# Kernel tuning notes

Hardware: AMD Instinct MI355X
Metric: run time of the kernel (lower is better)

The kernel has to match this reference:

```python
import jax, jax.numpy as jnp
import numpy as np

RAD = 4   # corr lookup radius
NH, NP = 8, 4  # deform attn heads / points (single level)


def conv2d(x, w, b, pad):
    y = jax.lax.conv_general_dilated(x, w, (1, 1), [(pad, pad), (pad, pad)],
                                     dimension_numbers=('NCHW', 'OIHW', 'NCHW'))
    return y + b[None, :, None, None]


def bilinear_gather(imgf, H, W, px, py):
    # imgf: [N, C, H*W]; px, py: [N, P] pixel coords; zero padding (grid_sample 'zeros')
    x0 = jnp.floor(px); y0 = jnp.floor(py)
    wx = px - x0; wy = py - y0
    def tap(xi, yi, wt):
        valid = (xi >= 0) & (xi <= W - 1) & (yi >= 0) & (yi <= H - 1)
        idx = (jnp.clip(yi, 0, H - 1) * W + jnp.clip(xi, 0, W - 1)).astype(jnp.int32)
        v = jnp.take_along_axis(imgf, idx[:, None, :], axis=2)
        return v * (wt * valid)[:, None, :]
    return (tap(x0, y0, (1 - wx) * (1 - wy)) + tap(x0 + 1, y0, wx * (1 - wy))
            + tap(x0, y0 + 1, (1 - wx) * wy) + tap(x0 + 1, y0 + 1, wx * wy))


def sine_pos_embed(B, H, W, npf, temperature=10000.0):
    # PositionEmbeddingSine with normalize=True
    scale = 2.0 * np.pi; eps = 1e-6
    y = jnp.broadcast_to(jnp.arange(1, H + 1, dtype=jnp.float32)[:, None], (H, W))
    x = jnp.broadcast_to(jnp.arange(1, W + 1, dtype=jnp.float32)[None, :], (H, W))
    y = (y - 0.5) / (H + eps) * scale
    x = (x - 0.5) / (W + eps) * scale
    dim_t = temperature ** (2.0 * (jnp.arange(npf) // 2).astype(jnp.float32) / npf)
    px = x[..., None] / dim_t
    py = y[..., None] / dim_t
    px = jnp.stack([jnp.sin(px[..., 0::2]), jnp.cos(px[..., 1::2])], -1).reshape(H, W, npf)
    py = jnp.stack([jnp.sin(py[..., 0::2]), jnp.cos(py[..., 1::2])], -1).reshape(H, W, npf)
    pos = jnp.concatenate([py, px], -1)
    return jnp.broadcast_to(pos[None], (B, H, W, 2 * npf)).reshape(B, H * W, 2 * npf)


def layer_norm(x, g, b):
    m = x.mean(-1, keepdims=True)
    v = ((x - m) ** 2).mean(-1, keepdims=True)
    return (x - m) / jnp.sqrt(v + 1e-5) * g + b


def _forward(fmap1, fmap2, flow, wc1, bc1, wc2, bc2, wf1, bf1, wf2, bf2, wcf, bcf,
             wfh1, bfh1, wfh2, bfh2, w_off, b_off, w_aw, b_aw, w_val, b_val,
             w_out, b_out, ln1_g, ln1_b, w_ff1, b_ff1, w_ff2, b_ff2, ln2_g, ln2_b):
    B, C, H, W = fmap1.shape
    HW = H * W
    dh = C // NH
    relu = jax.nn.relu
    # ---- CorrBlock.corr: all-pairs correlation volume ----
    corr = jnp.einsum('bcq,bck->bqk', fmap1.reshape(B, C, HW), fmap2.reshape(B, C, HW))
    corr = corr / jnp.sqrt(jnp.asarray(C, jnp.float32))
    corrf = corr.reshape(B * HW, 1, HW)  # [B*HW, 1, H2*W2]
    # ---- correlation lookup at coords = base grid + flow (bilinear, align_corners=True) ----
    gy, gx = jnp.meshgrid(jnp.arange(H, dtype=jnp.float32),
                          jnp.arange(W, dtype=jnp.float32), indexing='ij')
    cx = (gx[None] + flow[:, 0]).reshape(B * HW)
    cy = (gy[None] + flow[:, 1]).reshape(B * HW)
    d = jnp.linspace(-RAD, RAD, 2 * RAD + 1)
    oy, ox = jnp.meshgrid(d, d, indexing='ij')  # RAFT quirk: delta[...,0]=dy, delta[...,1]=dx
    px = cx[:, None] + oy.reshape(-1)[None, :]
    py = cy[:, None] + ox.reshape(-1)[None, :]
    corr_feat = bilinear_gather(corrf, H, W, px, py).reshape(B, H, W, (2 * RAD + 1) ** 2)
    corr_feat = corr_feat.transpose(0, 3, 1, 2)  # [B, 81, H, W]
    # ---- BasicMotionEncoder + FlowHead (BasicUpdateBlock.forward path) ----
    cor = relu(conv2d(corr_feat, wc1, bc1, 0))
    cor = relu(conv2d(cor, wc2, bc2, 1))
    flo = relu(conv2d(flow, wf1, bf1, 3))
    flo = relu(conv2d(flo, wf2, bf2, 1))
    mf = relu(conv2d(jnp.concatenate([cor, flo], 1), wcf, bcf, 1))
    mf = jnp.concatenate([mf, flow], 1)  # [B,128,H,W]
    delta_flow = conv2d(relu(conv2d(mf, wfh1, bfh1, 1)), wfh2, bfh2, 1)  # [B,2,H,W]
    # ---- single-level MSDeformAttn encoder layer over fmap1 tokens ----
    src = fmap1.reshape(B, C, HW).transpose(0, 2, 1)  # [B, Lq, C]
    pos = sine_pos_embed(B, H, W, C // 2)
    q = src + pos
    off = (q @ w_off.T + b_off).reshape(B, HW, NH, 1, NP, 2)
    aw = jax.nn.softmax((q @ w_aw.T + b_aw).reshape(B, HW, NH, NP), axis=-1)
    val = (src @ w_val.T + b_val).reshape(B, HW, NH, dh)
    ref = jnp.stack([(gx.reshape(-1) + 0.5) / W, (gy.reshape(-1) + 0.5) / H], -1)  # [HW,2]
    loc = (ref[None, :, None, None, None, :] + off / jnp.asarray([W, H], jnp.float32))[:, :, :, 0]
    # normalized loc -> pixel coords with align_corners=False convention
    px2 = (loc[..., 0] * W - 0.5).transpose(0, 2, 1, 3).reshape(B * NH, HW * NP)
    py2 = (loc[..., 1] * H - 0.5).transpose(0, 2, 1, 3).reshape(B * NH, HW * NP)
    vflat = val.transpose(0, 2, 3, 1).reshape(B * NH, dh, HW)
    samp = bilinear_gather(vflat, H, W, px2, py2).reshape(B, NH, dh, HW, NP)
    attn = (samp * aw.transpose(0, 2, 1, 3)[:, :, None]).sum(-1)  # [B,NH,dh,HW]
    attn = attn.transpose(0, 3, 1, 2).reshape(B, HW, C) @ w_out.T + b_out
    src = layer_norm(src + attn, ln1_g, ln1_b)
    ff = jax.nn.relu(src @ w_ff1.T + b_ff1) @ w_ff2.T + b_ff2
    src = layer_norm(src + ff, ln2_g, ln2_b)
    return src, delta_flow


def setup_inputs():
    key = jax.random.key(0)
    ks = jax.random.split(key, 20)
    B, C, H, W = 4, 256, 48, 48
    def w(i, shape, s=0.02):
        return jax.random.normal(ks[i], shape, jnp.float32) * s
    return {
        'fmap1': jax.random.normal(ks[0], (B, C, H, W), jnp.float32),
        'fmap2': jax.random.normal(ks[1], (B, C, H, W), jnp.float32),
        'flow': jax.random.normal(ks[2], (B, 2, H, W), jnp.float32),
        'wc1': w(3, (256, 81, 1, 1)), 'bc1': jnp.zeros((256,)),
        'wc2': w(4, (192, 256, 3, 3)), 'bc2': jnp.zeros((192,)),
        'wf1': w(5, (128, 2, 7, 7)), 'bf1': jnp.zeros((128,)),
        'wf2': w(6, (64, 128, 3, 3)), 'bf2': jnp.zeros((64,)),
        'wcf': w(7, (126, 256, 3, 3)), 'bcf': jnp.zeros((126,)),
        'wfh1': w(8, (256, 128, 3, 3)), 'bfh1': jnp.zeros((256,)),
        'wfh2': w(9, (2, 256, 3, 3)), 'bfh2': jnp.zeros((2,)),
        'w_off': w(10, (64, 256)), 'b_off': jnp.zeros((64,)),
        'w_aw': w(11, (32, 256)), 'b_aw': jnp.zeros((32,)),
        'w_val': w(12, (256, 256)), 'b_val': jnp.zeros((256,)),
        'w_out': w(13, (256, 256)), 'b_out': jnp.zeros((256,)),
        'ln1_g': jnp.ones((256,)), 'ln1_b': jnp.zeros((256,)),
        'w_ff1': w(14, (1024, 256)), 'b_ff1': jnp.zeros((1024,)),
        'w_ff2': w(15, (256, 1024)), 'b_ff2': jnp.zeros((256,)),
        'ln2_g': jnp.ones((256,)), 'ln2_b': jnp.zeros((256,)),
    }


def reference(fmap1, fmap2, flow, wc1, bc1, wc2, bc2, wf1, bf1, wf2, bf2, wcf, bcf,
              wfh1, bfh1, wfh2, bfh2, w_off, b_off, w_aw, b_aw, w_val, b_val,
              w_out, b_out, ln1_g, ln1_b, w_ff1, b_ff1, w_ff2, b_ff2, ln2_g, ln2_b):
    return _forward(fmap1, fmap2, flow, wc1, bc1, wc2, bc2, wf1, bf1, wf2, bf2, wcf, bcf,
                    wfh1, bfh1, wfh2, bfh2, w_off, b_off, w_aw, b_aw, w_val, b_val,
                    w_out, b_out, ln1_g, ln1_b, w_ff1, b_ff1, w_ff2, b_ff2, ln2_g, ln2_b)
```

## Files before the change

### kernel.cpp

```cpp
#include <hip/hip_runtime.h>
#include <hip/hip_bf16.h>
#include <math.h>

#define HH 48
#define WW 48
#define HW 2304
#define BB 4
#define CC 256

typedef __hip_bfloat16 bf16;
typedef __attribute__((ext_vector_type(8))) short s8v;
typedef __attribute__((ext_vector_type(4))) float f4v;

__device__ inline float bf2f(short u) {
  unsigned v = ((unsigned)(unsigned short)u) << 16;
  return __builtin_bit_cast(float, v);
}

__global__ __launch_bounds__(256) void prep_k(const float* __restrict__ fmap1,
                                              const float* __restrict__ fmap2,
                                              float* __restrict__ srcT,
                                              bf16* __restrict__ f1t,
                                              bf16* __restrict__ qb,
                                              bf16* __restrict__ f2t) {
  __shared__ float t[64][65];
  int z = blockIdx.z;
  int p0 = blockIdx.x * 64, c0 = blockIdx.y * 64;
  int b = z & 3;
  const float* src = (z < 4) ? fmap2 : fmap1;
  const float* inb = src + ((size_t)b * CC + c0) * HW + p0;
#pragma unroll
  for (int i = 0; i < 16; ++i) {
    int idx = threadIdx.x + i * 256;
    int c = idx >> 6, p = idx & 63;
    t[c][p] = inb[(size_t)c * HW + p];
  }
  __syncthreads();
  if (z < 4) {
    bf16* ob = f2t + ((size_t)b * HW + p0) * 256 + c0;
#pragma unroll
    for (int i = 0; i < 16; ++i) {
      int idx = threadIdx.x + i * 256;
      int p = idx >> 6, c = idx & 63;
      ob[(size_t)p * 256 + c] = (bf16)t[c][p];
    }
  } else {
    const float TWO_PI = 6.283185307179586f;
#pragma unroll
    for (int i = 0; i < 16; ++i) {
      int idx = threadIdx.x + i * 256;
      int pl = idx >> 6, cl = idx & 63;
      int c = c0 + cl;
      int p = p0 + pl;
      int y = p / WW, x = p % WW;
      float s = t[cl][pl];
      int axis = c >> 7;
      int cc = c & 127;
      int mm = cc >> 1;
      float coord = (axis ? ((float)x + 0.5f) : ((float)y + 0.5f)) * (TWO_PI / (48.f + 1e-6f));
      float tp = exp2f((float)mm * (13.287712379549449f / 64.f));
      float a = coord / tp;
      float pv = (cc & 1) ? cosf(a) : sinf(a);
      size_t o = ((size_t)b * HW + p) * 256 + c;
      srcT[o] = s;
      f1t[o] = (bf16)s;
      qb[o] = (bf16)(s + pv);
    }
  }
}

__global__ __launch_bounds__(256) void fused_corr_k(const bf16* __restrict__ f1t,
                                                    const bf16* __restrict__ f2t,
                                                    const float* __restrict__ flow,
                                                    bf16* __restrict__ cf) {
  __shared__ float Dls[4][112];
  int wave = threadIdx.x >> 6, lane = threadIdx.x & 63;
  int q = blockIdx.x * 4 + wave;
  int b = q / HW, p = q - b * HW;
  int y = p / WW, x = p - y * WW;
  float fx = flow[((size_t)b * 2 + 0) * HW + p];
  float fy = flow[((size_t)b * 2 + 1) * HW + p];
  float sx = (float)x + fx, sy = (float)y + fy;
  float fx0 = floorf(sx), fy0 = floorf(sy);
  int ix0 = (int)fx0, iy0 = (int)fy0;
  float wx = sx - fx0, wy = sy - fy0;
  int fl = lane & 15, fk8 = lane >> 4;
  s8v bfrag[8];
  const bf16* f1q = f1t + (size_t)q * 256;
#pragma unroll
  for (int ks = 0; ks < 8; ++ks) bfrag[ks] = *(const s8v*)(f1q + ks * 32 + fk8 * 8);
  const bf16* rowp[7];
#pragma unroll
  for (int g = 0; g < 7; ++g) {
    int w = g * 16 + fl;
    int jy = w / 10, jx = w - jy * 10;
    int ky = iy0 - 4 + jy, kx = ix0 - 4 + jx;
    bool valid = (w < 100) && ((unsigned)kx < (unsigned)WW) && ((unsigned)ky < (unsigned)HH);
    rowp[g] = valid ? (f2t + ((size_t)b * HW + ky * WW + kx) * 256) : nullptr;
  }
  f4v acc[7] = {};
#pragma unroll
  for (int g = 0; g < 7; ++g) {
#pragma unroll
    for (int ks = 0; ks < 8; ++ks) {
      s8v a = {0, 0, 0, 0, 0, 0, 0, 0};
      if (rowp[g]) a = *(const s8v*)(rowp[g] + ks * 32 + fk8 * 8);
      acc[g] = __builtin_amdgcn_mfma_f32_16x16x32_bf16(a, bfrag[ks], acc[g], 0, 0, 0);
    }
  }
  if (fl == 0) {
#pragma unroll
    for (int g = 0; g < 7; ++g)
#pragma unroll
      for (int r = 0; r < 4; ++r)
        Dls[wave][g * 16 + fk8 * 4 + r] = acc[g][r] * 0.0625f;
  }
  __syncthreads();
  float w00 = (1.f - wx) * (1.f - wy), w10 = wx * (1.f - wy);
  float w01 = (1.f - wx) * wy, w11 = wx * wy;
  const float* D = Dls[wave];
  bf16* cfr = cf + (size_t)q * 96;
  for (int t = lane; t < 96; t += 64) {
    float v = 0.f;
    if (t < 81) {
      int jx = t / 9, jy = t - jx * 9;
      v = w00 * D[jy * 10 + jx] + w10 * D[jy * 10 + jx + 1] +
          w01 * D[(jy + 1) * 10 + jx] + w11 * D[(jy + 1) * 10 + jx + 1];
    }
    cfr[t] = (bf16)v;
  }
}

struct WtSegs {
  const float* src[12];
  unsigned dstOff[12];
  int Cout[12], Cin[12], KP[12], KS2[12];
  unsigned cum[13];
};

__global__ __launch_bounds__(256) void wt_all_k(WtSegs s, bf16* __restrict__ base) {
  unsigned idx = blockIdx.x * 256 + threadIdx.x;
  if (idx >= s.cum[12]) return;
  int seg = 0;
#pragma unroll
  for (int i = 1; i < 12; ++i)
    if (idx >= s.cum[i]) seg = i;
  unsigned r = idx - s.cum[seg];
  int KP = s.KP[seg], Cout = s.Cout[seg], Cin = s.Cin[seg], KS2 = s.KS2[seg];
  int c = r % KP;
  int o = (r / KP) % Cout;
  int t = r / (KP * Cout);
  float v;
  if (KS2 == 0) {
    int cc = c >> 6, tt = c & 63;
    v = (tt < 49) ? s.src[seg][((size_t)o * 2 + cc) * 49 + tt] : 0.f;
  } else {
    v = (c < Cin) ? s.src[seg][((size_t)o * Cin + c) * KS2 + t] : 0.f;
  }
  base[s.dstOff[seg] + r] = (bf16)v;
}

__global__ __launch_bounds__(256) void im2col7_k(const float* __restrict__ flow,
                                                 bf16* __restrict__ col7) {
  int g = blockIdx.x * 256 + threadIdx.x;
  int kp = g & 127;
  int n = g >> 7;
  int b = n / HW;
  int p = n % HW;
  int y = p / WW, x = p % WW;
  int cc = kp >> 6, tt = kp & 63;
  float v = 0.f;
  if (tt < 49) {
    int ky = tt / 7, kx = tt % 7;
    int yy = y + ky - 3, xx = x + kx - 3;
    if ((unsigned)yy < (unsigned)HH && (unsigned)xx < (unsigned)WW)
      v = flow[((size_t)b * 2 + cc) * HW + yy * WW + xx];
  }
  col7[g] = (bf16)v;
}

struct GSegs {
  const bf16* in[4];
  const bf16* wt[4];
  const float* bias[4];
  const float* bias2[4];
  float* outf[4];
  bf16* outb[4];
  int split[4], O[4], KP[4], taps[4], OStride[4], OOff[4], relu[4], nTn[4];
  int blkStart[4];
  int nseg;
};

__global__ __launch_bounds__(256) void gemm_group_k(GSegs s) {
  int blk = blockIdx.x;
  int seg = 0;
#pragma unroll
  for (int i = 1; i < 4; ++i)
    if (i < s.nseg && blk >= s.blkStart[i]) seg = i;
  int rel = blk - s.blkStart[seg];
  int nTn = s.nTn[seg];
  int bm = rel / nTn, bn = rel % nTn;
  int m0 = bm * 128, n0 = bn * 64;
  int KP = s.KP[seg], O = s.O[seg], taps = s.taps[seg];
  const bf16* in = s.in[seg];
  const bf16* wt = s.wt[seg];

  __shared__ short As[2][128][64];
  __shared__ short Bs[2][64][64];
  int tid = threadIdx.x;
  int arl = tid >> 1, asl = (tid & 1) * 4;
  int brl = tid >> 2, bsl = (tid & 3) * 2;
  int wave = tid >> 6, lane = tid & 63;
  int wm = (wave >> 1) * 64, wn = (wave & 1) * 32;
  int fl = lane & 15, fk8 = lane >> 4;
  f4v acc[4][2] = {};
  int m = m0 + arl;
  int b = m / HW;
  int p = m - b * HW;
  int y = p / WW, x = p - y * WW;
  int wo = n0 + brl;
  bool wvalid = wo < O;
  int wo_c = wvalid ? wo : 0;

  int nc0 = (KP + 63) >> 6;
  int S = taps * nc0;
  uint4 apre[4], bpre[2];

  auto load_stage = [&](int st) {
    int t = st / nc0;
    int c0 = (st - t * nc0) * 64;
    int yy = y, xx = x;
    bool valid = true;
    if (taps == 9) {
      int ky = t / 3, kx = t - ky * 3;
      yy = y + ky - 1;
      xx = x + kx - 1;
      valid = ((unsigned)yy < (unsigned)HH) & ((unsigned)xx < (unsigned)WW);
    }
    const bf16* arow = in + ((size_t)b * HW + yy * WW + xx) * KP;
    const bf16* wrow = wt + ((size_t)t * O + wo_c) * KP;
#pragma unroll
    for (int q = 0; q < 4; ++q) {
      int col = c0 + (asl + q) * 8;
      uint4 v = {0u, 0u, 0u, 0u};
      if (valid && col < KP) v = *(const uint4*)(arow + col);
      apre[q] = v;
    }
#pragma unroll
    for (int q = 0; q < 2; ++q) {
      int col = c0 + (bsl + q) * 8;
      uint4 v = {0u, 0u, 0u, 0u};
      if (wvalid && col < KP) v = *(const uint4*)(wrow + col);
      bpre[q] = v;
    }
  };

  load_stage(0);
  int cur = 0;
  for (int st = 0; st < S; ++st) {
#pragma unroll
    for (int q = 0; q < 4; ++q) {
      int sr = asl + q;
      *(uint4*)&As[cur][arl][((sr ^ (arl & 7))) * 8] = apre[q];
    }
#pragma unroll
    for (int q = 0; q < 2; ++q) {
      int sr = bsl + q;
      *(uint4*)&Bs[cur][brl][((sr ^ (brl & 7))) * 8] = bpre[q];
    }
    if (st + 1 < S) load_stage(st + 1);
    __syncthreads();
#pragma unroll
    for (int cc = 0; cc < 2; ++cc) {
      s8v af[4], bfr[2];
#pragma unroll
      for (int i = 0; i < 4; ++i) {
        int ar = wm + i * 16 + fl;
        af[i] = *(const s8v*)&As[cur][ar][(((cc * 4 + fk8) ^ (ar & 7))) * 8];
      }
#pragma unroll
      for (int j = 0; j < 2; ++j) {
        int br = wn + j * 16 + fl;
        bfr[j] = *(const s8v*)&Bs[cur][br][(((cc * 4 + fk8) ^ (br & 7))) * 8];
      }
#pragma unroll
      for (int i = 0; i < 4; ++i)
#pragma unroll
        for (int j = 0; j < 2; ++j)
          acc[i][j] = __builtin_amdgcn_mfma_f32_16x16x32_bf16(af[i], bfr[j], acc[i][j], 0, 0, 0);
    }
    cur ^= 1;
  }
  int OStride = s.OStride[seg], OOff = s.OOff[seg], relu = s.relu[seg], split = s.split[seg];
  const float* bias = s.bias[seg];
  const float* bias2 = s.bias2[seg];
  float* outf = s.outf[seg];
  bf16* outb = s.outb[seg];
#pragma unroll
  for (int j = 0; j < 2; ++j) {
    int o = n0 + wn + j * 16 + fl;
    if (o < O) {
      float bsv = (bias2 != nullptr && o >= split) ? bias2[o - split] : bias[o];
#pragma unroll
      for (int i = 0; i < 4; ++i)
#pragma unroll
        for (int r = 0; r < 4; ++r) {
          int mm = m0 + wm + i * 16 + fk8 * 4 + r;
          float v = acc[i][j][r] + bsv;
          if (relu) v = fmaxf(v, 0.f);
          if (outb) outb[(size_t)mm * OStride + OOff + o] = (bf16)v;
          else outf[(size_t)mm * OStride + OOff + o] = v;
        }
    }
  }
}

__global__ __launch_bounds__(256) void convfh2_k(const bf16* __restrict__ fh1,
                                                 const float* __restrict__ w,
                                                 const float* __restrict__ bias,
                                                 float* __restrict__ out) {
  __shared__ float wl[4608];
  int tid = threadIdx.x;
#pragma unroll
  for (int i = tid; i < 4608; i += 256) {
    int o2 = i & 1;
    int t = (i >> 1) % 9;
    int c = i / 18;
    wl[i] = w[((size_t)o2 * 256 + c) * 9 + t];
  }
  __syncthreads();
  int wave = tid >> 6, lane = tid & 63;
  int pix = blockIdx.x * 4 + wave;
  int b = pix / HW;
  int q = pix % HW;
  int y = q / WW, x = q % WW;
  int c0 = lane * 4;
  float a0 = 0.f, a1 = 0.f;
#pragma unroll
  for (int ky = 0; ky < 3; ++ky) {
    int yy = y + ky - 1;
    if ((unsigned)yy >= (unsigned)HH) continue;
#pragma unroll
    for (int kx = 0; kx < 3; ++kx) {
      int xx = x + kx - 1;
      if ((unsigned)xx >= (unsigned)WW) continue;
      int t = ky * 3 + kx;
      const bf16* row = fh1 + ((size_t)b * HW + yy * WW + xx) * 256 + c0;
      ushort4 v = *(const ushort4*)row;
      unsigned short vv[4] = {v.x, v.y, v.z, v.w};
#pragma unroll
      for (int j = 0; j < 4; ++j) {
        float fv = bf2f((short)vv[j]);
        float2 wp = *(const float2*)&wl[((c0 + j) * 9 + t) * 2];
        a0 += fv * wp.x;
        a1 += fv * wp.y;
      }
    }
  }
#pragma unroll
  for (int offl = 32; offl > 0; offl >>= 1) {
    a0 += __shfl_xor(a0, offl);
    a1 += __shfl_xor(a1, offl);
  }
  if (lane == 0) {
    out[(size_t)b * 2 * HW + q] = a0 + bias[0];
    out[((size_t)b * 2 + 1) * HW + q] = a1 + bias[1];
  }
}

__global__ void copy_flow_k(const float* __restrict__ flow, bf16* __restrict__ mf) {
  int g = blockIdx.x * 256 + threadIdx.x;
  int p = g % HW;
  int c = (g / HW) % 2;
  int b = g / (2 * HW);
  mf[((size_t)b * HW + p) * 128 + 126 + c] = (bf16)flow[g];
}

__global__ __launch_bounds__(256) void deform_k(const float* __restrict__ val,
                                                const float* __restrict__ oa,
                                                bf16* __restrict__ attn) {
  int g = blockIdx.x * 256 + threadIdx.x;
  int d = g & 31;
  int nh = g >> 5;
  int h = nh & 7;
  int n = nh >> 3;
  int b = n / HW;
  int p = n % HW;
  int y = p / WW, x = p % WW;
  const float* ap = oa + (size_t)n * 96 + 64 + h * 4;
  float l0 = ap[0], l1 = ap[1], l2 = ap[2], l3 = ap[3];
  float mx = fmaxf(fmaxf(l0, l1), fmaxf(l2, l3));
  float e0 = expf(l0 - mx), e1 = expf(l1 - mx), e2 = expf(l2 - mx), e3 = expf(l3 - mx);
  float inv = 1.f / (e0 + e1 + e2 + e3);
  float wts[4] = {e0 * inv, e1 * inv, e2 * inv, e3 * inv};
  const float* offp = oa + (size_t)n * 96 + h * 8;
  const float* vb = val + (size_t)b * HW * 256 + h * 32 + d;
  float acc = 0.f;
#pragma unroll
  for (int pt = 0; pt < 4; ++pt) {
    float ox = offp[pt * 2 + 0];
    float oy = offp[pt * 2 + 1];
    float w = wts[pt];
    float px = (float)x + ox, py = (float)y + oy;
    float x0f = floorf(px), y0f = floorf(py);
    int x0 = (int)x0f, y0 = (int)y0f;
    float wx = px - x0f, wy = py - y0f;
    float s = 0.f;
    if ((unsigned)x0 < WW && (unsigned)y0 < HH)
      s += vb[(size_t)(y0 * WW + x0) * 256] * (1.f - wx) * (1.f - wy);
    if ((unsigned)(x0 + 1) < WW && (unsigned)y0 < HH)
      s += vb[(size_t)(y0 * WW + x0 + 1) * 256] * wx * (1.f - wy);
    if ((unsigned)x0 < WW && (unsigned)(y0 + 1) < HH)
      s += vb[(size_t)((y0 + 1) * WW + x0) * 256] * (1.f - wx) * wy;
    if ((unsigned)(x0 + 1) < WW && (unsigned)(y0 + 1) < HH)
      s += vb[(size_t)((y0 + 1) * WW + x0 + 1) * 256] * wx * wy;
    acc += w * s;
  }
  attn[(size_t)n * 256 + h * 32 + d] = (bf16)acc;
}

__global__ __launch_bounds__(256) void ln_add_k(const float* __restrict__ A,
                                                const float* __restrict__ Bv,
                                                const float* __restrict__ g,
                                                const float* __restrict__ be,
                                                float* __restrict__ out,
                                                bf16* __restrict__ outb) {
  int n = blockIdx.x;
  int c = threadIdx.x;
  float v = A[(size_t)n * 256 + c] + Bv[(size_t)n * 256 + c];
  float s1 = v, s2 = v * v;
#pragma unroll
  for (int o = 32; o > 0; o >>= 1) {
    s1 += __shfl_down(s1, o);
    s2 += __shfl_down(s2, o);
  }
  __shared__ float r1[4], r2[4], mv[2];
  int wid = c >> 6, lane = c & 63;
  if (lane == 0) {
    r1[wid] = s1;
    r2[wid] = s2;
  }
  __syncthreads();
  if (c == 0) {
    float a = r1[0] + r1[1] + r1[2] + r1[3];
    float q2 = r2[0] + r2[1] + r2[2] + r2[3];
    float mean = a * (1.f / 256.f);
    mv[0] = mean;
    mv[1] = q2 * (1.f / 256.f) - mean * mean;
  }
  __syncthreads();
  float mean = mv[0], var = mv[1];
  float r = (v - mean) * rsqrtf(var + 1e-5f) * g[c] + be[c];
  out[(size_t)n * 256 + c] = r;
  if (outb) outb[(size_t)n * 256 + c] = (bf16)r;
}

extern "C" void kernel_launch(void* const* d_in, const int* in_sizes, int n_in,
                              void* d_out, int out_size, void* d_ws, size_t ws_size,
                              hipStream_t stream) {
  const float* fmap1 = (const float*)d_in[0];
  const float* fmap2 = (const float*)d_in[1];
  const float* flow = (const float*)d_in[2];
  const float* wc1 = (const float*)d_in[3];
  const float* bc1 = (const float*)d_in[4];
  const float* wc2 = (const float*)d_in[5];
  const float* bc2 = (const float*)d_in[6];
  const float* wf1 = (const float*)d_in[7];
  const float* bf1 = (const float*)d_in[8];
  const float* wf2 = (const float*)d_in[9];
  const float* bf2 = (const float*)d_in[10];
  const float* wcf = (const float*)d_in[11];
  const float* bcf = (const float*)d_in[12];
  const float* wfh1 = (const float*)d_in[13];
  const float* bfh1 = (const float*)d_in[14];
  const float* wfh2 = (const float*)d_in[15];
  const float* bfh2 = (const float*)d_in[16];
  const float* w_off = (const float*)d_in[17];
  const float* b_off = (const float*)d_in[18];
  const float* w_aw = (const float*)d_in[19];
  const float* b_aw = (const float*)d_in[20];
  const float* w_val = (const float*)d_in[21];
  const float* b_val = (const float*)d_in[22];
  const float* w_out = (const float*)d_in[23];
  const float* b_out = (const float*)d_in[24];
  const float* ln1_g = (const float*)d_in[25];
  const float* ln1_b = (const float*)d_in[26];
  const float* w_ff1 = (const float*)d_in[27];
  const float* b_ff1 = (const float*)d_in[28];
  const float* w_ff2 = (const float*)d_in[29];
  const float* b_ff2 = (const float*)d_in[30];
  const float* ln2_g = (const float*)d_in[31];
  const float* ln2_b = (const float*)d_in[32];

  float* ws = (float*)d_ws;
  float* out_src = (float*)d_out;
  float* out_df = out_src + (size_t)BB * HW * CC;

  const size_t F_WT = 0;
  const size_t F_F1T = 11700000;
  const size_t F_F2T = 12900000;
  const size_t F_QB = 14100000;
  const size_t F_SRCT = 15300000;
  const size_t F_CF = 17700000;
  const size_t F_COL7 = 18200000;
  const size_t F_COR1 = 18800000;
  const size_t F_FLO1 = 20000000;
  const size_t F_CAT = 20600000;
  const size_t F_MF = 21800000;
  const size_t F_FH1 = 22400000;
  const size_t F_OA = 23600000;
  const size_t F_VAL = 24500000;
  const size_t F_ATTN = 26900000;
  const size_t F_TMP = 28100000;
  const size_t F_SRC1 = 30500000;
  const size_t F_SRC1B = 32900000;
  const size_t F_FF1 = 34100000;
  const size_t F_FF2 = 38900000;

  bf16* wkbase = (bf16*)(ws + F_WT);
  bf16* wk1 = wkbase + 0;
  bf16* wk2 = wkbase + 24576;
  bf16* wkf2 = wkbase + 466944;
  bf16* wkcf = wkbase + 540672;
  bf16* wkfh1 = wkbase + 830976;
  bf16* wl_oa = wkbase + 1125888;
  bf16* wl_val = wkbase + 1150464;
  bf16* wl_out = wkbase + 1216000;
  bf16* wl_ff1 = wkbase + 1281536;
  bf16* wl_ff2 = wkbase + 1543680;
  bf16* wk7 = wkbase + 1805824;
  bf16* f1t = (bf16*)(ws + F_F1T);
  bf16* f2t = (bf16*)(ws + F_F2T);
  bf16* qb = (bf16*)(ws + F_QB);
  bf16* cf = (bf16*)(ws + F_CF);
  bf16* col7 = (bf16*)(ws + F_COL7);
  bf16* cor1 = (bf16*)(ws + F_COR1);
  bf16* flo1 = (bf16*)(ws + F_FLO1);
  bf16* cat = (bf16*)(ws + F_CAT);
  bf16* mf = (bf16*)(ws + F_MF);
  bf16* fh1 = (bf16*)(ws + F_FH1);
  bf16* attnb = (bf16*)(ws + F_ATTN);
  bf16* src1b = (bf16*)(ws + F_SRC1B);
  bf16* ff1b = (bf16*)(ws + F_FF1);

  WtSegs segs;
  const float* srcs[12] = {wc1, wc2, wf2, wcf, wfh1, w_off, w_aw, w_val, w_out, w_ff1, w_ff2, wf1};
  unsigned offs[12] = {0, 24576, 466944, 540672, 830976, 1125888, 1142272, 1150464, 1216000, 1281536, 1543680, 1805824};
  int couts[12] = {256, 192, 64, 126, 256, 64, 32, 256, 256, 1024, 256, 128};
  int cins[12] = {81, 256, 128, 256, 128, 256, 256, 256, 256, 256, 1024, 2};
  int kps[12] = {96, 256, 128, 256, 128, 256, 256, 256, 256, 256, 1024, 128};
  int ks2[12] = {1, 9, 9, 9, 9, 1, 1, 1, 1, 1, 1, 0};
  unsigned cum = 0;
  for (int i = 0; i < 12; ++i) {
    segs.src[i] = srcs[i];
    segs.dstOff[i] = offs[i];
    segs.Cout[i] = couts[i];
    segs.Cin[i] = cins[i];
    segs.KP[i] = kps[i];
    segs.KS2[i] = ks2[i];
    segs.cum[i] = cum;
    cum += (unsigned)((ks2[i] ? ks2[i] : 1) * couts[i] * kps[i]);
  }
  segs.cum[12] = cum;
  wt_all_k<<<dim3((cum + 255) / 256), 256, 0, stream>>>(segs, wkbase);

  prep_k<<<dim3(36, 4, 8), 256, 0, stream>>>(fmap1, fmap2, ws + F_SRCT, f1t, qb, f2t);
  im2col7_k<<<dim3(4608), 256, 0, stream>>>(flow, col7);
  copy_flow_k<<<dim3(72), 256, 0, stream>>>(flow, mf);

  fused_corr_k<<<dim3(2304), 256, 0, stream>>>(f1t, f2t, flow, cf);

  auto setseg = [](GSegs& G, int i, const bf16* in, const bf16* wt, const float* bias,
                   const float* bias2, int split, float* outf, bf16* outb, int O, int KP,
                   int taps, int OStride, int OOff, int relu) {
    G.in[i] = in; G.wt[i] = wt; G.bias[i] = bias; G.bias2[i] = bias2; G.split[i] = split;
    G.outf[i] = outf; G.outb[i] = outb; G.O[i] = O; G.KP[i] = KP; G.taps[i] = taps;
    G.OStride[i] = OStride; G.OOff[i] = OOff; G.relu[i] = relu;
    G.nTn[i] = (O + 63) / 64;
  };
  auto finseg = [](GSegs& G, int n) {
    int cumb = 0;
    for (int i = 0; i < 4; ++i) {
      if (i < n) { G.blkStart[i] = cumb; cumb += G.nTn[i] * 72; }
      else G.blkStart[i] = 0x7fffffff;
    }
    G.nseg = n;
    return cumb;
  };

  GSegs GA;
  setseg(GA, 0, cf, wk1, bc1, nullptr, 1 << 30, nullptr, cor1, 256, 96, 1, 256, 0, 1);
  setseg(GA, 1, col7, wk7, bf1, nullptr, 1 << 30, nullptr, flo1, 128, 128, 1, 128, 0, 1);
  setseg(GA, 2, qb, wl_oa, b_off, b_aw, 64, ws + F_OA, nullptr, 96, 256, 1, 96, 0, 0);
  setseg(GA, 3, f1t, wl_val, b_val, nullptr, 1 << 30, ws + F_VAL, nullptr, 256, 256, 1, 256, 0, 0);
  int nblkA = finseg(GA, 4);
  gemm_group_k<<<dim3(nblkA), 256, 0, stream>>>(GA);

  deform_k<<<dim3(9216), 256, 0, stream>>>(ws + F_VAL, ws + F_OA, attnb);

  GSegs GB;
  setseg(GB, 0, cor1, wk2, bc2, nullptr, 1 << 30, nullptr, cat, 192, 256, 9, 256, 0, 1);
  setseg(GB, 1, flo1, wkf2, bf2, nullptr, 1 << 30, nullptr, cat, 64, 128, 9, 256, 192, 1);
  setseg(GB, 2, attnb, wl_out, b_out, nullptr, 1 << 30, ws + F_TMP, nullptr, 256, 256, 1, 256, 0, 0);
  int nblkB = finseg(GB, 3);
  gemm_group_k<<<dim3(nblkB), 256, 0, stream>>>(GB);

  ln_add_k<<<dim3(9216), 256, 0, stream>>>(ws + F_TMP, ws + F_SRCT, ln1_g, ln1_b, ws + F_SRC1, src1b);

  GSegs GC;
  setseg(GC, 0, cat, wkcf, bcf, nullptr, 1 << 30, nullptr, mf, 126, 256, 9, 128, 0, 1);
  setseg(GC, 1, src1b, wl_ff1, b_ff1, nullptr, 1 << 30, nullptr, ff1b, 1024, 256, 1, 1024, 0, 1);
  int nblkC = finseg(GC, 2);
  gemm_group_k<<<dim3(nblkC), 256, 0, stream>>>(GC);

  GSegs GD;
  setseg(GD, 0, mf, wkfh1, bfh1, nullptr, 1 << 30, nullptr, fh1, 256, 128, 9, 256, 0, 1);
  setseg(GD, 1, ff1b, wl_ff2, b_ff2, nullptr, 1 << 30, ws + F_FF2, nullptr, 256, 1024, 1, 256, 0, 0);
  int nblkD = finseg(GD, 2);
  gemm_group_k<<<dim3(nblkD), 256, 0, stream>>>(GD);

  convfh2_k<<<dim3(2304), 256, 0, stream>>>(fh1, wfh2, bfh2, out_df);
  ln_add_k<<<dim3(9216), 256, 0, stream>>>(ws + F_FF2, ws + F_SRC1, ln2_g, ln2_b, out_src, nullptr);

  (void)in_sizes; (void)n_in; (void)out_size; (void)ws_size;
}
```

Baseline: 277.1 us.

## Fold correlation into grouped GEMM launch and reschedule GEMM segments across stages

Removes the standalone correlation kernel and appends its blocks to the first grouped GEMM launch, so the corr lookup runs concurrently with the flow conv, offset/attention and value projections. The corr1 GEMM moves to the second launch, and the grouped GEMMs are regrouped into five launches following the dependency chain. The corr inner loop is also changed to double-buffer its f2 fragment loads ahead of the MFMAs. The extra launch and the uneven mix of block types within a launch may offset the gain from the overlap.

```diff
diff --git a/kernel.cpp b/kernel.cpp
--- a/kernel.cpp
+++ b/kernel.cpp
@@ -69,68 +69,6 @@
   }
 }
 
-__global__ __launch_bounds__(256) void fused_corr_k(const bf16* __restrict__ f1t,
-                                                    const bf16* __restrict__ f2t,
-                                                    const float* __restrict__ flow,
-                                                    bf16* __restrict__ cf) {
-  __shared__ float Dls[4][112];
-  int wave = threadIdx.x >> 6, lane = threadIdx.x & 63;
-  int q = blockIdx.x * 4 + wave;
-  int b = q / HW, p = q - b * HW;
-  int y = p / WW, x = p - y * WW;
-  float fx = flow[((size_t)b * 2 + 0) * HW + p];
-  float fy = flow[((size_t)b * 2 + 1) * HW + p];
-  float sx = (float)x + fx, sy = (float)y + fy;
-  float fx0 = floorf(sx), fy0 = floorf(sy);
-  int ix0 = (int)fx0, iy0 = (int)fy0;
-  float wx = sx - fx0, wy = sy - fy0;
-  int fl = lane & 15, fk8 = lane >> 4;
-  s8v bfrag[8];
-  const bf16* f1q = f1t + (size_t)q * 256;
-#pragma unroll
-  for (int ks = 0; ks < 8; ++ks) bfrag[ks] = *(const s8v*)(f1q + ks * 32 + fk8 * 8);
-  const bf16* rowp[7];
-#pragma unroll
-  for (int g = 0; g < 7; ++g) {
-    int w = g * 16 + fl;
-    int jy = w / 10, jx = w - jy * 10;
-    int ky = iy0 - 4 + jy, kx = ix0 - 4 + jx;
-    bool valid = (w < 100) && ((unsigned)kx < (unsigned)WW) && ((unsigned)ky < (unsigned)HH);
-    rowp[g] = valid ? (f2t + ((size_t)b * HW + ky * WW + kx) * 256) : nullptr;
-  }
-  f4v acc[7] = {};
-#pragma unroll
-  for (int g = 0; g < 7; ++g) {
-#pragma unroll
-    for (int ks = 0; ks < 8; ++ks) {
-      s8v a = {0, 0, 0, 0, 0, 0, 0, 0};
-      if (rowp[g]) a = *(const s8v*)(rowp[g] + ks * 32 + fk8 * 8);
-      acc[g] = __builtin_amdgcn_mfma_f32_16x16x32_bf16(a, bfrag[ks], acc[g], 0, 0, 0);
-    }
-  }
-  if (fl == 0) {
-#pragma unroll
-    for (int g = 0; g < 7; ++g)
-#pragma unroll
-      for (int r = 0; r < 4; ++r)
-        Dls[wave][g * 16 + fk8 * 4 + r] = acc[g][r] * 0.0625f;
-  }
-  __syncthreads();
-  float w00 = (1.f - wx) * (1.f - wy), w10 = wx * (1.f - wy);
-  float w01 = (1.f - wx) * wy, w11 = wx * wy;
-  const float* D = Dls[wave];
-  bf16* cfr = cf + (size_t)q * 96;
-  for (int t = lane; t < 96; t += 64) {
-    float v = 0.f;
-    if (t < 81) {
-      int jx = t / 9, jy = t - jx * 9;
-      v = w00 * D[jy * 10 + jx] + w10 * D[jy * 10 + jx + 1] +
-          w01 * D[(jy + 1) * 10 + jx] + w11 * D[(jy + 1) * 10 + jx + 1];
-    }
-    cfr[t] = (bf16)v;
-  }
-}
-
 struct WtSegs {
   const float* src[12];
   unsigned dstOff[12];
@@ -191,7 +129,86 @@
   int nseg;
 };
 
-__global__ __launch_bounds__(256) void gemm_group_k(GSegs s) {
+__global__ __launch_bounds__(256) void mega_k(GSegs s, int corrStart,
+                                              const bf16* __restrict__ f1t,
+                                              const bf16* __restrict__ f2t,
+                                              const float* __restrict__ flow,
+                                              bf16* __restrict__ cf) {
+  __shared__ short As[2][128][64];
+  __shared__ short Bs[2][64][64];
+
+  if ((int)blockIdx.x >= corrStart) {
+    int cb = blockIdx.x - corrStart;
+    int wave = threadIdx.x >> 6, lane = threadIdx.x & 63;
+    int q = cb * 4 + wave;
+    int b = q / HW, p = q - b * HW;
+    int y = p / WW, x = p - y * WW;
+    float fx = flow[((size_t)b * 2 + 0) * HW + p];
+    float fy = flow[((size_t)b * 2 + 1) * HW + p];
+    float sx = (float)x + fx, sy = (float)y + fy;
+    float fx0 = floorf(sx), fy0 = floorf(sy);
+    int ix0 = (int)fx0, iy0 = (int)fy0;
+    float wx = sx - fx0, wy = sy - fy0;
+    int fl = lane & 15, fk8 = lane >> 4;
+    s8v bfrag[8];
+    const bf16* f1q = f1t + (size_t)q * 256;
+#pragma unroll
+    for (int ks = 0; ks < 8; ++ks) bfrag[ks] = *(const s8v*)(f1q + ks * 32 + fk8 * 8);
+    const bf16* rowp[7];
+#pragma unroll
+    for (int g = 0; g < 7; ++g) {
+      int w = g * 16 + fl;
+      int jy = w / 10, jx = w - jy * 10;
+      int ky = iy0 - 4 + jy, kx = ix0 - 4 + jx;
+      bool valid = (w < 100) && ((unsigned)kx < (unsigned)WW) && ((unsigned)ky < (unsigned)HH);
+      rowp[g] = valid ? (f2t + ((size_t)b * HW + ky * WW + kx) * 256) : nullptr;
+    }
+    f4v acc[7] = {};
+    s8v af[2][7];
+#pragma unroll
+    for (int g = 0; g < 7; ++g) {
+      s8v a = {0, 0, 0, 0, 0, 0, 0, 0};
+      if (rowp[g]) a = *(const s8v*)(rowp[g] + fk8 * 8);
+      af[0][g] = a;
+    }
+#pragma unroll
+    for (int ks = 0; ks < 8; ++ks) {
+      if (ks < 7) {
+#pragma unroll
+        for (int g = 0; g < 7; ++g) {
+          s8v a = {0, 0, 0, 0, 0, 0, 0, 0};
+          if (rowp[g]) a = *(const s8v*)(rowp[g] + (ks + 1) * 32 + fk8 * 8);
+          af[(ks + 1) & 1][g] = a;
+        }
+      }
+#pragma unroll
+      for (int g = 0; g < 7; ++g)
+        acc[g] = __builtin_amdgcn_mfma_f32_16x16x32_bf16(af[ks & 1][g], bfrag[ks], acc[g], 0, 0, 0);
+    }
+    float* Dls = ((float*)As) + wave * 112;
+    if (fl == 0) {
+#pragma unroll
+      for (int g = 0; g < 7; ++g)
+#pragma unroll
+        for (int r = 0; r < 4; ++r)
+          Dls[g * 16 + fk8 * 4 + r] = acc[g][r] * 0.0625f;
+    }
+    __syncthreads();
+    float w00 = (1.f - wx) * (1.f - wy), w10 = wx * (1.f - wy);
+    float w01 = (1.f - wx) * wy, w11 = wx * wy;
+    bf16* cfr = cf + (size_t)q * 96;
+    for (int t = lane; t < 96; t += 64) {
+      float v = 0.f;
+      if (t < 81) {
+        int jx = t / 9, jy = t - jx * 9;
+        v = w00 * Dls[jy * 10 + jx] + w10 * Dls[jy * 10 + jx + 1] +
+            w01 * Dls[(jy + 1) * 10 + jx] + w11 * Dls[(jy + 1) * 10 + jx + 1];
+      }
+      cfr[t] = (bf16)v;
+    }
+    return;
+  }
+
   int blk = blockIdx.x;
   int seg = 0;
 #pragma unroll
@@ -205,8 +222,6 @@
   const bf16* in = s.in[seg];
   const bf16* wt = s.wt[seg];
 
-  __shared__ short As[2][128][64];
-  __shared__ short Bs[2][64][64];
   int tid = threadIdx.x;
   int arl = tid >> 1, asl = (tid & 1) * 4;
   int brl = tid >> 2, bsl = (tid & 3) * 2;
@@ -272,11 +287,11 @@
     __syncthreads();
 #pragma unroll
     for (int cc = 0; cc < 2; ++cc) {
-      s8v af[4], bfr[2];
+      s8v af2[4], bfr[2];
 #pragma unroll
       for (int i = 0; i < 4; ++i) {
         int ar = wm + i * 16 + fl;
-        af[i] = *(const s8v*)&As[cur][ar][(((cc * 4 + fk8) ^ (ar & 7))) * 8];
+        af2[i] = *(const s8v*)&As[cur][ar][(((cc * 4 + fk8) ^ (ar & 7))) * 8];
       }
 #pragma unroll
       for (int j = 0; j < 2; ++j) {
@@ -287,7 +302,7 @@
       for (int i = 0; i < 4; ++i)
 #pragma unroll
         for (int j = 0; j < 2; ++j)
-          acc[i][j] = __builtin_amdgcn_mfma_f32_16x16x32_bf16(af[i], bfr[j], acc[i][j], 0, 0, 0);
+          acc[i][j] = __builtin_amdgcn_mfma_f32_16x16x32_bf16(af2[i], bfr[j], acc[i][j], 0, 0, 0);
     }
     cur ^= 1;
   }
@@ -568,8 +583,6 @@
   im2col7_k<<<dim3(4608), 256, 0, stream>>>(flow, col7);
   copy_flow_k<<<dim3(72), 256, 0, stream>>>(flow, mf);
 
-  fused_corr_k<<<dim3(2304), 256, 0, stream>>>(f1t, f2t, flow, cf);
-
   auto setseg = [](GSegs& G, int i, const bf16* in, const bf16* wt, const float* bias,
                    const float* bias2, int split, float* outf, bf16* outb, int O, int KP,
                    int taps, int OStride, int OOff, int relu) {
@@ -587,37 +600,42 @@
     G.nseg = n;
     return cumb;
   };
-
-  GSegs GA;
-  setseg(GA, 0, cf, wk1, bc1, nullptr, 1 << 30, nullptr, cor1, 256, 96, 1, 256, 0, 1);
-  setseg(GA, 1, col7, wk7, bf1, nullptr, 1 << 30, nullptr, flo1, 128, 128, 1, 128, 0, 1);
-  setseg(GA, 2, qb, wl_oa, b_off, b_aw, 64, ws + F_OA, nullptr, 96, 256, 1, 96, 0, 0);
-  setseg(GA, 3, f1t, wl_val, b_val, nullptr, 1 << 30, ws + F_VAL, nullptr, 256, 256, 1, 256, 0, 0);
-  int nblkA = finseg(GA, 4);
-  gemm_group_k<<<dim3(nblkA), 256, 0, stream>>>(GA);
+  const int BIG = 1 << 30;
+
+  GSegs M1;
+  setseg(M1, 0, col7, wk7, bf1, nullptr, BIG, nullptr, flo1, 128, 128, 1, 128, 0, 1);
+  setseg(M1, 1, qb, wl_oa, b_off, b_aw, 64, ws + F_OA, nullptr, 96, 256, 1, 96, 0, 0);
+  setseg(M1, 2, f1t, wl_val, b_val, nullptr, BIG, ws + F_VAL, nullptr, 256, 256, 1, 256, 0, 0);
+  int nblk1 = finseg(M1, 3);
+  mega_k<<<dim3(nblk1 + 2304), 256, 0, stream>>>(M1, nblk1, f1t, f2t, flow, cf);
 
   deform_k<<<dim3(9216), 256, 0, stream>>>(ws + F_VAL, ws + F_OA, attnb);
 
-  GSegs GB;
-  setseg(GB, 0, cor1, wk2, bc2, nullptr, 1 << 30, nullptr, cat, 192, 256, 9, 256, 0, 1);
-  setseg(GB, 1, flo1, wkf2, bf2, nullptr, 1 << 30, nullptr, cat, 64, 128, 9, 256, 192, 1);
-  setseg(GB, 2, attnb, wl_out, b_out, nullptr, 1 << 30, ws + F_TMP, nullptr, 256, 256, 1, 256, 0, 0);
-  int nblkB = finseg(GB, 3);
-  gemm_group_k<<<dim3(nblkB), 256, 0, stream>>>(GB);
+  GSegs M2;
+  setseg(M2, 0, cf, wk1, bc1, nullptr, BIG, nullptr, cor1, 256, 96, 1, 256, 0, 1);
+  setseg(M2, 1, flo1, wkf2, bf2, nullptr, BIG, nullptr, cat, 64, 128, 9, 256, 192, 1);
+  setseg(M2, 2, attnb, wl_out, b_out, nullptr, BIG, ws + F_TMP, nullptr, 256, 256, 1, 256, 0, 0);
+  int nblk2 = finseg(M2, 3);
+  mega_k<<<dim3(nblk2), 256, 0, stream>>>(M2, BIG, f1t, f2t, flow, cf);
 
   ln_add_k<<<dim3(9216), 256, 0, stream>>>(ws + F_TMP, ws + F_SRCT, ln1_g, ln1_b, ws + F_SRC1, src1b);
 
-  GSegs GC;
-  setseg(GC, 0, cat, wkcf, bcf, nullptr, 1 << 30, nullptr, mf, 126, 256, 9, 128, 0, 1);
-  setseg(GC, 1, src1b, wl_ff1, b_ff1, nullptr, 1 << 30, nullptr, ff1b, 1024, 256, 1, 1024, 0, 1);
-  int nblkC = finseg(GC, 2);
-  gemm_group_k<<<dim3(nblkC), 256, 0, stream>>>(GC);
-
-  GSegs GD;
-  setseg(GD, 0, mf, wkfh1, bfh1, nullptr, 1 << 30, nullptr, fh1, 256, 128, 9, 256, 0, 1);
-  setseg(GD, 1, ff1b, wl_ff2, b_ff2, nullptr, 1 << 30, ws + F_FF2, nullptr, 256, 1024, 1, 256, 0, 0);
-  int nblkD = finseg(GD, 2);
-  gemm_group_k<<<dim3(nblkD), 256, 0, stream>>>(GD);
+  GSegs M3;
+  setseg(M3, 0, cor1, wk2, bc2, nullptr, BIG, nullptr, cat, 192, 256, 9, 256, 0, 1);
+  setseg(M3, 1, src1b, wl_ff1, b_ff1, nullptr, BIG, nullptr, ff1b, 1024, 256, 1, 1024, 0, 1);
+  int nblk3 = finseg(M3, 2);
+  mega_k<<<dim3(nblk3), 256, 0, stream>>>(M3, BIG, f1t, f2t, flow, cf);
+
+  GSegs M4;
+  setseg(M4, 0, cat, wkcf, bcf, nullptr, BIG, nullptr, mf, 126, 256, 9, 128, 0, 1);
+  setseg(M4, 1, ff1b, wl_ff2, b_ff2, nullptr, BIG, ws + F_FF2, nullptr, 256, 1024, 1, 256, 0, 0);
+  int nblk4 = finseg(M4, 2);
+  mega_k<<<dim3(nblk4), 256, 0, stream>>>(M4, BIG, f1t, f2t, flow, cf);
+
+  GSegs M5;
+  setseg(M5, 0, mf, wkfh1, bfh1, nullptr, BIG, nullptr, fh1, 256, 128, 9, 256, 0, 1);
+  int nblk5 = finseg(M5, 1);
+  mega_k<<<dim3(nblk5), 256, 0, stream>>>(M5, BIG, f1t, f2t, flow, cf);
 
   convfh2_k<<<dim3(2304), 256, 0, stream>>>(fh1, wfh2, bfh2, out_df);
   ln_add_k<<<dim3(9216), 256, 0, stream>>>(ws + F_FF2, ws + F_SRC1, ln2_g, ln2_b, out_src, nullptr);
```

New measurement: 277.9 us. Within noise of the previous version (+0.3%).

## Split correlation K across waves per pixel and store value projection in bf16

Applied to the files above, without the earlier changes.

The correlation kernel now gives one block per query pixel, with each of the four waves handling a 64-channel slice of K. All loads are issued up front, and the partial dot products are reduced through shared memory before the bilinear 9x9 lookup. This raises parallelism and memory-level concurrency over the old one-wave-per-pixel, eight-step serial MFMA chain, at the cost of an extra sync and reduction. Separately, the value projection GEMM writes bf16 instead of fp32, and deform_k reads bf16, which halves gather traffic but lowers value precision.

```diff
diff --git a/kernel.cpp b/kernel.cpp
--- a/kernel.cpp
+++ b/kernel.cpp
@@ -73,9 +73,10 @@
                                                     const bf16* __restrict__ f2t,
                                                     const float* __restrict__ flow,
                                                     bf16* __restrict__ cf) {
-  __shared__ float Dls[4][112];
+  __shared__ float Dp[4][112];
+  __shared__ float Ds[112];
+  int q = blockIdx.x;
   int wave = threadIdx.x >> 6, lane = threadIdx.x & 63;
-  int q = blockIdx.x * 4 + wave;
   int b = q / HW, p = q - b * HW;
   int y = p / WW, x = p - y * WW;
   float fx = flow[((size_t)b * 2 + 0) * HW + p];
@@ -85,10 +86,9 @@
   int ix0 = (int)fx0, iy0 = (int)fy0;
   float wx = sx - fx0, wy = sy - fy0;
   int fl = lane & 15, fk8 = lane >> 4;
-  s8v bfrag[8];
-  const bf16* f1q = f1t + (size_t)q * 256;
-#pragma unroll
-  for (int ks = 0; ks < 8; ++ks) bfrag[ks] = *(const s8v*)(f1q + ks * 32 + fk8 * 8);
+  const bf16* f1q = f1t + (size_t)q * 256 + wave * 64;
+  s8v bf0 = *(const s8v*)(f1q + fk8 * 8);
+  s8v bf1v = *(const s8v*)(f1q + 32 + fk8 * 8);
   const bf16* rowp[7];
 #pragma unroll
   for (int g = 0; g < 7; ++g) {
@@ -96,38 +96,47 @@
     int jy = w / 10, jx = w - jy * 10;
     int ky = iy0 - 4 + jy, kx = ix0 - 4 + jx;
     bool valid = (w < 100) && ((unsigned)kx < (unsigned)WW) && ((unsigned)ky < (unsigned)HH);
-    rowp[g] = valid ? (f2t + ((size_t)b * HW + ky * WW + kx) * 256) : nullptr;
+    rowp[g] = valid ? (f2t + ((size_t)b * HW + ky * WW + kx) * 256 + wave * 64) : nullptr;
+  }
+  s8v a0[7], a1[7];
+#pragma unroll
+  for (int g = 0; g < 7; ++g) {
+    s8v z = {0, 0, 0, 0, 0, 0, 0, 0};
+    a0[g] = rowp[g] ? *(const s8v*)(rowp[g] + fk8 * 8) : z;
+  }
+#pragma unroll
+  for (int g = 0; g < 7; ++g) {
+    s8v z = {0, 0, 0, 0, 0, 0, 0, 0};
+    a1[g] = rowp[g] ? *(const s8v*)(rowp[g] + 32 + fk8 * 8) : z;
   }
   f4v acc[7] = {};
 #pragma unroll
-  for (int g = 0; g < 7; ++g) {
-#pragma unroll
-    for (int ks = 0; ks < 8; ++ks) {
-      s8v a = {0, 0, 0, 0, 0, 0, 0, 0};
-      if (rowp[g]) a = *(const s8v*)(rowp[g] + ks * 32 + fk8 * 8);
-      acc[g] = __builtin_amdgcn_mfma_f32_16x16x32_bf16(a, bfrag[ks], acc[g], 0, 0, 0);
-    }
-  }
+  for (int g = 0; g < 7; ++g)
+    acc[g] = __builtin_amdgcn_mfma_f32_16x16x32_bf16(a0[g], bf0, acc[g], 0, 0, 0);
+#pragma unroll
+  for (int g = 0; g < 7; ++g)
+    acc[g] = __builtin_amdgcn_mfma_f32_16x16x32_bf16(a1[g], bf1v, acc[g], 0, 0, 0);
   if (fl == 0) {
 #pragma unroll
     for (int g = 0; g < 7; ++g)
 #pragma unroll
       for (int r = 0; r < 4; ++r)
-        Dls[wave][g * 16 + fk8 * 4 + r] = acc[g][r] * 0.0625f;
+        Dp[wave][g * 16 + fk8 * 4 + r] = acc[g][r];
   }
   __syncthreads();
-  float w00 = (1.f - wx) * (1.f - wy), w10 = wx * (1.f - wy);
-  float w01 = (1.f - wx) * wy, w11 = wx * wy;
-  const float* D = Dls[wave];
-  bf16* cfr = cf + (size_t)q * 96;
-  for (int t = lane; t < 96; t += 64) {
+  int tid = threadIdx.x;
+  if (tid < 112) Ds[tid] = (Dp[0][tid] + Dp[1][tid] + Dp[2][tid] + Dp[3][tid]) * 0.0625f;
+  __syncthreads();
+  if (tid < 96) {
+    float w00 = (1.f - wx) * (1.f - wy), w10 = wx * (1.f - wy);
+    float w01 = (1.f - wx) * wy, w11 = wx * wy;
     float v = 0.f;
-    if (t < 81) {
-      int jx = t / 9, jy = t - jx * 9;
-      v = w00 * D[jy * 10 + jx] + w10 * D[jy * 10 + jx + 1] +
-          w01 * D[(jy + 1) * 10 + jx] + w11 * D[(jy + 1) * 10 + jx + 1];
-    }
-    cfr[t] = (bf16)v;
+    if (tid < 81) {
+      int jx = tid / 9, jy = tid - jx * 9;
+      v = w00 * Ds[jy * 10 + jx] + w10 * Ds[jy * 10 + jx + 1] +
+          w01 * Ds[(jy + 1) * 10 + jx] + w11 * Ds[(jy + 1) * 10 + jx + 1];
+    }
+    cf[(size_t)q * 96 + tid] = (bf16)v;
   }
 }
 
@@ -240,18 +249,18 @@
     const bf16* arow = in + ((size_t)b * HW + yy * WW + xx) * KP;
     const bf16* wrow = wt + ((size_t)t * O + wo_c) * KP;
 #pragma unroll
-    for (int q = 0; q < 4; ++q) {
-      int col = c0 + (asl + q) * 8;
+    for (int qq = 0; qq < 4; ++qq) {
+      int col = c0 + (asl + qq) * 8;
       uint4 v = {0u, 0u, 0u, 0u};
       if (valid && col < KP) v = *(const uint4*)(arow + col);
-      apre[q] = v;
-    }
-#pragma unroll
-    for (int q = 0; q < 2; ++q) {
-      int col = c0 + (bsl + q) * 8;
+      apre[qq] = v;
+    }
+#pragma unroll
+    for (int qq = 0; qq < 2; ++qq) {
+      int col = c0 + (bsl + qq) * 8;
       uint4 v = {0u, 0u, 0u, 0u};
       if (wvalid && col < KP) v = *(const uint4*)(wrow + col);
-      bpre[q] = v;
+      bpre[qq] = v;
     }
   };
 
@@ -259,14 +268,14 @@
   int cur = 0;
   for (int st = 0; st < S; ++st) {
 #pragma unroll
-    for (int q = 0; q < 4; ++q) {
-      int sr = asl + q;
-      *(uint4*)&As[cur][arl][((sr ^ (arl & 7))) * 8] = apre[q];
-    }
-#pragma unroll
-    for (int q = 0; q < 2; ++q) {
-      int sr = bsl + q;
-      *(uint4*)&Bs[cur][brl][((sr ^ (brl & 7))) * 8] = bpre[q];
+    for (int qq = 0; qq < 4; ++qq) {
+      int sr = asl + qq;
+      *(uint4*)&As[cur][arl][((sr ^ (arl & 7))) * 8] = apre[qq];
+    }
+#pragma unroll
+    for (int qq = 0; qq < 2; ++qq) {
+      int sr = bsl + qq;
+      *(uint4*)&Bs[cur][brl][((sr ^ (brl & 7))) * 8] = bpre[qq];
     }
     if (st + 1 < S) load_stage(st + 1);
     __syncthreads();
@@ -376,7 +385,7 @@
   mf[((size_t)b * HW + p) * 128 + 126 + c] = (bf16)flow[g];
 }
 
-__global__ __launch_bounds__(256) void deform_k(const float* __restrict__ val,
+__global__ __launch_bounds__(256) void deform_k(const bf16* __restrict__ val,
                                                 const float* __restrict__ oa,
                                                 bf16* __restrict__ attn) {
   int g = blockIdx.x * 256 + threadIdx.x;
@@ -394,7 +403,7 @@
   float inv = 1.f / (e0 + e1 + e2 + e3);
   float wts[4] = {e0 * inv, e1 * inv, e2 * inv, e3 * inv};
   const float* offp = oa + (size_t)n * 96 + h * 8;
-  const float* vb = val + (size_t)b * HW * 256 + h * 32 + d;
+  const bf16* vb = val + (size_t)b * HW * 256 + h * 32 + d;
   float acc = 0.f;
 #pragma unroll
   for (int pt = 0; pt < 4; ++pt) {
@@ -407,13 +416,13 @@
     float wx = px - x0f, wy = py - y0f;
     float s = 0.f;
     if ((unsigned)x0 < WW && (unsigned)y0 < HH)
-      s += vb[(size_t)(y0 * WW + x0) * 256] * (1.f - wx) * (1.f - wy);
+      s += (float)vb[(size_t)(y0 * WW + x0) * 256] * (1.f - wx) * (1.f - wy);
     if ((unsigned)(x0 + 1) < WW && (unsigned)y0 < HH)
-      s += vb[(size_t)(y0 * WW + x0 + 1) * 256] * wx * (1.f - wy);
+      s += (float)vb[(size_t)(y0 * WW + x0 + 1) * 256] * wx * (1.f - wy);
     if ((unsigned)x0 < WW && (unsigned)(y0 + 1) < HH)
-      s += vb[(size_t)((y0 + 1) * WW + x0) * 256] * (1.f - wx) * wy;
+      s += (float)vb[(size_t)((y0 + 1) * WW + x0) * 256] * (1.f - wx) * wy;
     if ((unsigned)(x0 + 1) < WW && (unsigned)(y0 + 1) < HH)
-      s += vb[(size_t)((y0 + 1) * WW + x0 + 1) * 256] * wx * wy;
+      s += (float)vb[(size_t)((y0 + 1) * WW + x0 + 1) * 256] * wx * wy;
     acc += w * s;
   }
   attn[(size_t)n * 256 + h * 32 + d] = (bf16)acc;
@@ -539,6 +548,7 @@
   bf16* cat = (bf16*)(ws + F_CAT);
   bf16* mf = (bf16*)(ws + F_MF);
   bf16* fh1 = (bf16*)(ws + F_FH1);
+  bf16* valb = (bf16*)(ws + F_VAL);
   bf16* attnb = (bf16*)(ws + F_ATTN);
   bf16* src1b = (bf16*)(ws + F_SRC1B);
   bf16* ff1b = (bf16*)(ws + F_FF1);
@@ -568,7 +578,7 @@
   im2col7_k<<<dim3(4608), 256, 0, stream>>>(flow, col7);
   copy_flow_k<<<dim3(72), 256, 0, stream>>>(flow, mf);
 
-  fused_corr_k<<<dim3(2304), 256, 0, stream>>>(f1t, f2t, flow, cf);
+  fused_corr_k<<<dim3(9216), 256, 0, stream>>>(f1t, f2t, flow, cf);
 
   auto setseg = [](GSegs& G, int i, const bf16* in, const bf16* wt, const float* bias,
                    const float* bias2, int split, float* outf, bf16* outb, int O, int KP,
@@ -587,35 +597,36 @@
     G.nseg = n;
     return cumb;
   };
+  const int BIG = 1 << 30;
 
   GSegs GA;
-  setseg(GA, 0, cf, wk1, bc1, nullptr, 1 << 30, nullptr, cor1, 256, 96, 1, 256, 0, 1);
-  setseg(GA, 1, col7, wk7, bf1, nullptr, 1 << 30, nullptr, flo1, 128, 128, 1, 128, 0, 1);
+  setseg(GA, 0, cf, wk1, bc1, nullptr, BIG, nullptr, cor1, 256, 96, 1, 256, 0, 1);
+  setseg(GA, 1, col7, wk7, bf1, nullptr, BIG, nullptr, flo1, 128, 128, 1, 128, 0, 1);
   setseg(GA, 2, qb, wl_oa, b_off, b_aw, 64, ws + F_OA, nullptr, 96, 256, 1, 96, 0, 0);
-  setseg(GA, 3, f1t, wl_val, b_val, nullptr, 1 << 30, ws + F_VAL, nullptr, 256, 256, 1, 256, 0, 0);
+  setseg(GA, 3, f1t, wl_val, b_val, nullptr, BIG, nullptr, valb, 256, 256, 1, 256, 0, 0);
   int nblkA = finseg(GA, 4);
   gemm_group_k<<<dim3(nblkA), 256, 0, stream>>>(GA);
 
-  deform_k<<<dim3(9216), 256, 0, stream>>>(ws + F_VAL, ws + F_OA, attnb);
+  deform_k<<<dim3(9216), 256, 0, stream>>>(valb, ws + F_OA, attnb);
 
   GSegs GB;
-  setseg(GB, 0, cor1, wk2, bc2, nullptr, 1 << 30, nullptr, cat, 192, 256, 9, 256, 0, 1);
-  setseg(GB, 1, flo1, wkf2, bf2, nullptr, 1 << 30, nullptr, cat, 64, 128, 9, 256, 192, 1);
-  setseg(GB, 2, attnb, wl_out, b_out, nullptr, 1 << 30, ws + F_TMP, nullptr, 256, 256, 1, 256, 0, 0);
+  setseg(GB, 0, cor1, wk2, bc2, nullptr, BIG, nullptr, cat, 192, 256, 9, 256, 0, 1);
+  setseg(GB, 1, flo1, wkf2, bf2, nullptr, BIG, nullptr, cat, 64, 128, 9, 256, 192, 1);
+  setseg(GB, 2, attnb, wl_out, b_out, nullptr, BIG, ws + F_TMP, nullptr, 256, 256, 1, 256, 0, 0);
   int nblkB = finseg(GB, 3);
   gemm_group_k<<<dim3(nblkB), 256, 0, stream>>>(GB);
 
   ln_add_k<<<dim3(9216), 256, 0, stream>>>(ws + F_TMP, ws + F_SRCT, ln1_g, ln1_b, ws + F_SRC1, src1b);
 
   GSegs GC;
-  setseg(GC, 0, cat, wkcf, bcf, nullptr, 1 << 30, nullptr, mf, 126, 256, 9, 128, 0, 1);
-  setseg(GC, 1, src1b, wl_ff1, b_ff1, nullptr, 1 << 30, nullptr, ff1b, 1024, 256, 1, 1024, 0, 1);
+  setseg(GC, 0, cat, wkcf, bcf, nullptr, BIG, nullptr, mf, 126, 256, 9, 128, 0, 1);
+  setseg(GC, 1, src1b, wl_ff1, b_ff1, nullptr, BIG, nullptr, ff1b, 1024, 256, 1, 1024, 0, 1);
   int nblkC = finseg(GC, 2);
   gemm_group_k<<<dim3(nblkC), 256, 0, stream>>>(GC);
 
   GSegs GD;
-  setseg(GD, 0, mf, wkfh1, bfh1, nullptr, 1 << 30, nullptr, fh1, 256, 128, 9, 256, 0, 1);
-  setseg(GD, 1, ff1b, wl_ff2, b_ff2, nullptr, 1 << 30, ws + F_FF2, nullptr, 256, 1024, 1, 256, 0, 0);
+  setseg(GD, 0, mf, wkfh1, bfh1, nullptr, BIG, nullptr, fh1, 256, 128, 9, 256, 0, 1);
+  setseg(GD, 1, ff1b, wl_ff2, b_ff2, nullptr, BIG, ws + F_FF2, nullptr, 256, 1024, 1, 256, 0, 0);
   int nblkD = finseg(GD, 2);
   gemm_group_k<<<dim3(nblkD), 256, 0, stream>>>(GD);
 
```

After: 266.3 us. -3.9%, faster.
